# Optimization experiments

Hardware: AMD Instinct MI355X
Metric: run time of the kernel (lower is better)

The kernel has to match this reference:

```python
import jax, jax.numpy as jnp
import numpy as np

SHAPE = (8, 16, 16)          # N-dim spatial shape, seq_len = 2048
DIM_Q = 512
DIM_KV = 512
N_HEAD = 8
N_LAYER = 8
D_K = DIM_Q // N_HEAD        # 64
D_V = DIM_KV // N_HEAD       # 64


def setup_inputs() -> dict:
    key = jax.random.key(0)
    ks = jax.random.split(key, 8)
    b = 2
    q = jax.random.normal(ks[0], (b, *SHAPE, DIM_Q), dtype=jnp.float32)
    k = jax.random.normal(ks[1], (b, *SHAPE, DIM_KV), dtype=jnp.float32)
    v = jax.random.normal(ks[2], (b, *SHAPE, DIM_KV), dtype=jnp.float32)
    # torch nn.Linear weights are [out, in]; we apply x @ W.T below
    Wq = jax.random.normal(ks[3], (N_HEAD * D_K, DIM_Q), dtype=jnp.float32) / np.sqrt(DIM_Q)
    Wk = jax.random.normal(ks[4], (N_HEAD * D_K, DIM_KV), dtype=jnp.float32) / np.sqrt(DIM_KV)
    Wv = jax.random.normal(ks[5], (N_HEAD * D_V, DIM_KV), dtype=jnp.float32) / np.sqrt(DIM_KV)
    Wo = jax.random.normal(ks[6], (DIM_Q, N_HEAD * D_V), dtype=jnp.float32) / np.sqrt(DIM_Q * N_LAYER)
    bo = jnp.zeros((DIM_Q,), dtype=jnp.float32)
    return {"q": q, "k": k, "v": v, "Wq": Wq, "Wk": Wk, "Wv": Wv, "Wo": Wo, "bo": bo}


def reference(q, k, v, Wq, Wk, Wv, Wo, bo):
    b = q.shape[0]
    spatial = q.shape[1:-1]                      # (8,16,16)
    n = int(np.prod(spatial))                    # 2048
    # flatten spatial dims -> [b, N, c]
    qf = q.reshape(b, n, -1)
    kf = k.reshape(b, n, -1)
    vf = v.reshape(b, n, -1)
    # QKV projections (nn.Linear, bias=False): x @ W.T
    qp = jnp.einsum('bnc,dc->bnd', qf, Wq)
    kp = jnp.einsum('bnc,dc->bnd', kf, Wk)
    vp = jnp.einsum('bnc,dc->bnd', vf, Wv)
    # split heads -> [b, h, N, d]
    qh = qp.reshape(b, n, N_HEAD, D_K).transpose(0, 2, 1, 3)
    kh = kp.reshape(b, n, N_HEAD, D_K).transpose(0, 2, 1, 3)
    vh = vp.reshape(b, n, N_HEAD, D_V).transpose(0, 2, 1, 3)
    # full attention with causal tril mask, scale 1/sqrt(d_k)
    scores = jnp.einsum('bhqd,bhkd->bhqk', qh, kh) / np.sqrt(D_K)
    causal = jnp.tril(jnp.ones((n, n), dtype=bool))
    scores = jnp.where(causal, scores, -jnp.inf)
    attn = jax.nn.softmax(scores, axis=-1)       # attn_dropout=0.0 -> identity
    a = jnp.einsum('bhqk,bhkd->bhqd', attn, vh)
    # merge heads -> [b, N, h*d_v]
    a = a.transpose(0, 2, 1, 3).reshape(b, n, N_HEAD * D_V)
    # output projection (bias=True)
    out = jnp.einsum('bnd,cd->bnc', a, Wo) + bo
    return out.reshape(b, *spatial, DIM_Q)
```

## Files before the change

kernel.cpp:

```cpp
#include <hip/hip_runtime.h>
#include <hip/hip_bf16.h>

typedef __bf16 bf16_t;
typedef __attribute__((ext_vector_type(4))) __bf16 bf16x4;
typedef __attribute__((ext_vector_type(8))) __bf16 bf16x8;
typedef __attribute__((ext_vector_type(4))) float f32x4;

#define MFMA16(a, b, c) __builtin_amdgcn_mfma_f32_16x16x32_bf16((a), (b), (c), 0, 0, 0)
#define EXP2(x) __builtin_amdgcn_exp2f(x)

constexpr int NB   = 2;
constexpr int NH   = 8;
constexpr int NSEQ = 2048;
constexpr int CD   = 512;
constexpr int DH   = 64;
constexpr int MTOK = NB * NSEQ;

__device__ __forceinline__ bf16_t f2b(float x) { return (bf16_t)x; }

__global__ __launch_bounds__(256) void qkv_proj_kernel(
    const float* __restrict__ Xq, const float* __restrict__ Xk, const float* __restrict__ Xv,
    const float* __restrict__ Wq, const float* __restrict__ Wk, const float* __restrict__ Wv,
    bf16_t* __restrict__ Qp, bf16_t* __restrict__ Kf, bf16_t* __restrict__ Vf)
{
    __shared__ bf16_t Xs[64][72];
    __shared__ bf16_t Ws[64][72];

    const int z = blockIdx.z;
    const float* __restrict__ X = (z == 0) ? Xq : (z == 1) ? Xk : Xv;
    const float* __restrict__ W = (z == 0) ? Wq : (z == 1) ? Wk : Wv;
    bf16_t* __restrict__ Out    = (z == 0) ? Qp : (z == 1) ? Kf : Vf;

    const int tid  = threadIdx.x;
    const int lane = tid & 63;
    const int wid  = tid >> 6;
    const int lrow = lane & 15;
    const int lk   = (lane >> 4) * 8;
    const int m0w  = (wid >> 1) * 32;
    const int n0w  = (wid & 1) * 32;
    const int bm   = blockIdx.x * 64;
    const int bn   = blockIdx.y * 64;

    const int srow = tid >> 4;
    const int sc4  = (tid & 15) * 4;

    f32x4 xg[4], wg[4];
    #pragma unroll
    for (int rr = 0; rr < 4; ++rr) {
        int r = rr * 16 + srow;
        xg[rr] = *reinterpret_cast<const f32x4*>(X + (size_t)(bm + r) * CD + sc4);
        wg[rr] = *reinterpret_cast<const f32x4*>(W + (size_t)(bn + r) * CD + sc4);
    }

    f32x4 acc[2][2] = {};
    for (int k0 = 0; k0 < CD; k0 += 64) {
        #pragma unroll
        for (int rr = 0; rr < 4; ++rr) {
            int r = rr * 16 + srow;
            bf16x4 xb, wb;
            #pragma unroll
            for (int c = 0; c < 4; ++c) { xb[c] = f2b(xg[rr][c]); wb[c] = f2b(wg[rr][c]); }
            *reinterpret_cast<bf16x4*>(&Xs[r][sc4]) = xb;
            *reinterpret_cast<bf16x4*>(&Ws[r][sc4]) = wb;
        }
        __syncthreads();

        if (k0 + 64 < CD) {
            #pragma unroll
            for (int rr = 0; rr < 4; ++rr) {
                int r = rr * 16 + srow;
                xg[rr] = *reinterpret_cast<const f32x4*>(X + (size_t)(bm + r) * CD + k0 + 64 + sc4);
                wg[rr] = *reinterpret_cast<const f32x4*>(W + (size_t)(bn + r) * CD + k0 + 64 + sc4);
            }
        }

        #pragma unroll
        for (int kk = 0; kk < 2; ++kk) {
            int o = kk * 32 + lk;
            bf16x8 a0 = *reinterpret_cast<const bf16x8*>(&Xs[m0w + lrow][o]);
            bf16x8 a1 = *reinterpret_cast<const bf16x8*>(&Xs[m0w + 16 + lrow][o]);
            bf16x8 b0 = *reinterpret_cast<const bf16x8*>(&Ws[n0w + lrow][o]);
            bf16x8 b1 = *reinterpret_cast<const bf16x8*>(&Ws[n0w + 16 + lrow][o]);
            acc[0][0] = MFMA16(a0, b0, acc[0][0]);
            acc[0][1] = MFMA16(a0, b1, acc[0][1]);
            acc[1][0] = MFMA16(a1, b0, acc[1][0]);
            acc[1][1] = MFMA16(a1, b1, acc[1][1]);
        }
        __syncthreads();
    }

    if (z == 0) {
        #pragma unroll
        for (int f = 0; f < 2; ++f)
            #pragma unroll
            for (int gg = 0; gg < 2; ++gg)
                #pragma unroll
                for (int j = 0; j < 4; ++j) {
                    int row = bm + m0w + f * 16 + (lane >> 4) * 4 + j;
                    int col = bn + n0w + gg * 16 + lrow;
                    int b = row >> 11, n = row & (NSEQ - 1);
                    int h = col >> 6,  d = col & (DH - 1);
                    Out[(((size_t)(b * NH + h) * NSEQ) + n) * DH + d] = f2b(acc[f][gg][j]);
                }
    } else if (z == 1) {
        #pragma unroll
        for (int f = 0; f < 2; ++f)
            #pragma unroll
            for (int gg = 0; gg < 2; ++gg) {
                int rowb = bm + m0w + f * 16 + (lane >> 4) * 4;
                int col  = bn + n0w + gg * 16 + lrow;
                int bq = rowb >> 11;
                int h = col >> 6, d = col & (DH - 1);
                bf16_t* hb = Out + (size_t)(bq * NH + h) * NSEQ * DH;
                #pragma unroll
                for (int j = 0; j < 4; ++j) {
                    int n = (rowb + j) & (NSEQ - 1);
                    hb[((size_t)(n >> 4) * 2 + (d >> 5)) * 512 +
                       ((d >> 3) & 3) * 128 + (n & 15) * 8 + (d & 7)] = f2b(acc[f][gg][j]);
                }
            }
    } else {
        #pragma unroll
        for (int f = 0; f < 2; ++f)
            #pragma unroll
            for (int gg = 0; gg < 2; ++gg) {
                int rowb = bm + m0w + f * 16 + (lane >> 4) * 4;
                int col  = bn + n0w + gg * 16 + lrow;
                int bq = rowb >> 11;
                int n0 = rowb & (NSEQ - 1);
                int h = col >> 6, dv = col & (DH - 1);
                bf16_t* hb = Out + (size_t)(bq * NH + h) * NSEQ * DH;
                bf16x4 pk;
                #pragma unroll
                for (int j = 0; j < 4; ++j) pk[j] = f2b(acc[f][gg][j]);
                *reinterpret_cast<bf16x4*>(
                    &hb[((size_t)(n0 >> 5) * 4 + (dv >> 4)) * 512 +
                        ((n0 >> 3) & 3) * 128 + (dv & 15) * 8 + (n0 & 7)]) = pk;
            }
    }
}

__device__ __forceinline__ void attn_qblock(
    const bf16_t* __restrict__ Q, const bf16_t* __restrict__ K,
    const bf16_t* __restrict__ V, bf16_t* __restrict__ Aout,
    int b, int h, int p, int tid,
    char (*wreg)[8704], float (*sl)[32])
{
    const int lane = tid & 63;
    const int w    = tid >> 6;
    const int r    = lane & 15;
    const int g    = lane >> 4;
    const int qb   = p * 32;

    bf16_t* Pl = (bf16_t*)wreg[w];

    const float QS = 0.125f * 1.4426950408889634f;
    const float MSHIFT = 16.f;
    bf16x8 qf[2][2];
    #pragma unroll
    for (int f = 0; f < 2; ++f)
        #pragma unroll
        for (int dh = 0; dh < 2; ++dh) {
            bf16x8 t = *reinterpret_cast<const bf16x8*>(
                Q + (size_t)(qb + f * 16 + r) * DH + dh * 32 + g * 8);
            #pragma unroll
            for (int i = 0; i < 8; ++i) qf[f][dh][i] = f2b((float)t[i] * QS);
        }

    float l0 = 0.f, l1 = 0.f;
    f32x4 O[2][4] = {};

    const int T = (p + 2) >> 1;

    bf16x8 kc[4][2];
    if (w < T) {
        #pragma unroll
        for (int kk = 0; kk < 4; ++kk)
            #pragma unroll
            for (int dh = 0; dh < 2; ++dh)
                kc[kk][dh] = *reinterpret_cast<const bf16x8*>(
                    K + (((size_t)(w * 4 + kk) * 2 + dh) * 64 + lane) * 8);
    }

    for (int c = w; c < T; c += 4) {
        const int kb = c * 64;

        bf16x8 bv[4][2];
        #pragma unroll
        for (int df = 0; df < 4; ++df)
            #pragma unroll
            for (int ks = 0; ks < 2; ++ks)
                bv[df][ks] = *reinterpret_cast<const bf16x8*>(
                    V + (((size_t)(c * 2 + ks) * 4 + df) * 64 + lane) * 8);

        f32x4 s[2][4] = {};
        __builtin_amdgcn_s_setprio(1);
        #pragma unroll
        for (int kk = 0; kk < 4; ++kk) {
            s[0][kk] = MFMA16(kc[kk][0], qf[0][0], s[0][kk]);
            s[0][kk] = MFMA16(kc[kk][1], qf[0][1], s[0][kk]);
            s[1][kk] = MFMA16(kc[kk][0], qf[1][0], s[1][kk]);
            s[1][kk] = MFMA16(kc[kk][1], qf[1][1], s[1][kk]);
        }
        __builtin_amdgcn_s_setprio(0);

        bf16x8 kn[4][2];
        const int cn = c + 4;
        if (cn < T) {
            #pragma unroll
            for (int kk = 0; kk < 4; ++kk)
                #pragma unroll
                for (int dh = 0; dh < 2; ++dh)
                    kn[kk][dh] = *reinterpret_cast<const bf16x8*>(
                        K + (((size_t)(cn * 4 + kk) * 2 + dh) * 64 + lane) * 8);
        }

        if (kb + 63 > qb) {
            #pragma unroll
            for (int f = 0; f < 2; ++f) {
                const int qg = qb + f * 16 + r;
                #pragma unroll
                for (int kk = 0; kk < 4; ++kk)
                    #pragma unroll
                    for (int j = 0; j < 4; ++j) {
                        int kg = kb + kk * 16 + g * 4 + j;
                        if (kg > qg) s[f][kk][j] = -1e30f;
                    }
            }
        }

        #pragma unroll
        for (int kk = 0; kk < 4; ++kk)
            #pragma unroll
            for (int j = 0; j < 4; ++j) {
                float e0 = EXP2(s[0][kk][j] - MSHIFT);
                float e1 = EXP2(s[1][kk][j] - MSHIFT);
                s[0][kk][j] = e0; l0 += e0;
                s[1][kk][j] = e1; l1 += e1;
            }

        #pragma unroll
        for (int f = 0; f < 2; ++f)
            #pragma unroll
            for (int kk = 0; kk < 4; ++kk) {
                bf16x4 pk4;
                #pragma unroll
                for (int j = 0; j < 4; ++j) pk4[j] = f2b(s[f][kk][j]);
                *reinterpret_cast<bf16x4*>(&Pl[(size_t)(f * 16 + r) * 72 + kk * 16 + g * 4]) = pk4;
            }
        asm volatile("s_waitcnt lgkmcnt(0)" ::: "memory");

        bf16x8 pa0l = *reinterpret_cast<const bf16x8*>(&Pl[(size_t)r * 72 + g * 8]);
        bf16x8 pa1l = *reinterpret_cast<const bf16x8*>(&Pl[(size_t)(16 + r) * 72 + g * 8]);
        bf16x8 pa0h = *reinterpret_cast<const bf16x8*>(&Pl[(size_t)r * 72 + 32 + g * 8]);
        bf16x8 pa1h = *reinterpret_cast<const bf16x8*>(&Pl[(size_t)(16 + r) * 72 + 32 + g * 8]);
        __builtin_amdgcn_s_setprio(1);
        #pragma unroll
        for (int df = 0; df < 4; ++df) {
            O[0][df] = MFMA16(pa0l, bv[df][0], O[0][df]);
            O[1][df] = MFMA16(pa1l, bv[df][0], O[1][df]);
            O[0][df] = MFMA16(pa0h, bv[df][1], O[0][df]);
            O[1][df] = MFMA16(pa1h, bv[df][1], O[1][df]);
        }
        __builtin_amdgcn_s_setprio(0);

        #pragma unroll
        for (int kk = 0; kk < 4; ++kk) { kc[kk][0] = kn[kk][0]; kc[kk][1] = kn[kk][1]; }
    }

    l0 += __shfl_xor(l0, 16);
    l1 += __shfl_xor(l1, 16);
    l0 += __shfl_xor(l0, 32);
    l1 += __shfl_xor(l1, 32);

    float* sO = (float*)wreg[w];
    #pragma unroll
    for (int f = 0; f < 2; ++f)
        #pragma unroll
        for (int df = 0; df < 4; ++df)
            #pragma unroll
            for (int j = 0; j < 4; ++j)
                sO[(size_t)(f * 16 + g * 4 + j) * 68 + df * 16 + r] = O[f][df][j];
    if (lane < 16) { sl[w][r] = l0; sl[w][16 + r] = l1; }
    __syncthreads();

    {
        const int row = tid >> 3;
        const int c0  = (tid & 7) * 8;
        float lstar = sl[0][row] + sl[1][row] + sl[2][row] + sl[3][row];
        f32x4 acc0 = {}, acc1 = {};
        #pragma unroll
        for (int w2 = 0; w2 < 4; ++w2) {
            const float* po = (const float*)wreg[w2] + (size_t)row * 68 + c0;
            f32x4 o0 = *reinterpret_cast<const f32x4*>(po);
            f32x4 o1 = *reinterpret_cast<const f32x4*>(po + 4);
            #pragma unroll
            for (int cc = 0; cc < 4; ++cc) { acc0[cc] += o0[cc]; acc1[cc] += o1[cc]; }
        }
        float inv = 1.f / lstar;
        bf16x8 pk;
        #pragma unroll
        for (int cc = 0; cc < 4; ++cc) { pk[cc] = f2b(acc0[cc] * inv); pk[4 + cc] = f2b(acc1[cc] * inv); }
        *reinterpret_cast<bf16x8*>(Aout + ((size_t)b * NSEQ + qb + row) * CD + h * DH + c0) = pk;
    }
    __syncthreads();
}

__global__ __launch_bounds__(256, 2) void attn_kernel(
    const bf16_t* __restrict__ Qp, const bf16_t* __restrict__ Kf,
    const bf16_t* __restrict__ Vf, bf16_t* __restrict__ Aout)
{
    __shared__ __align__(16) char wreg[4][8704];
    __shared__ float sl[4][32];

    const int tid = threadIdx.x;
    const int bh = blockIdx.x;
    const int b = bh >> 3, h = bh & 7;
    const int pp = blockIdx.y;

    const bf16_t* Q = Qp + (size_t)bh * NSEQ * DH;
    const bf16_t* K = Kf + (size_t)bh * NSEQ * DH;
    const bf16_t* V = Vf + (size_t)bh * NSEQ * DH;

    attn_qblock(Q, K, V, Aout, b, h, 63 - pp, tid, wreg, sl);
    attn_qblock(Q, K, V, Aout, b, h, pp,      tid, wreg, sl);
}

__global__ __launch_bounds__(256) void out_proj_kernel(
    const bf16_t* __restrict__ A, const float* __restrict__ Wo,
    const float* __restrict__ bo, float* __restrict__ Out)
{
    __shared__ bf16_t As[64][72];
    __shared__ bf16_t Ws[64][72];

    const int tid  = threadIdx.x;
    const int lane = tid & 63;
    const int wid  = tid >> 6;
    const int lrow = lane & 15;
    const int lk   = (lane >> 4) * 8;
    const int m0w  = (wid >> 1) * 32;
    const int n0w  = (wid & 1) * 32;
    const int bm   = blockIdx.x * 64;
    const int bn   = blockIdx.y * 64;

    const int srow = tid >> 4;
    const int sc4  = (tid & 15) * 4;

    bf16x4 ag[4];
    f32x4  wg[4];
    #pragma unroll
    for (int rr = 0; rr < 4; ++rr) {
        int r = rr * 16 + srow;
        ag[rr] = *reinterpret_cast<const bf16x4*>(A  + (size_t)(bm + r) * CD + sc4);
        wg[rr] = *reinterpret_cast<const f32x4*>(Wo + (size_t)(bn + r) * CD + sc4);
    }

    f32x4 acc[2][2] = {};
    for (int k0 = 0; k0 < CD; k0 += 64) {
        #pragma unroll
        for (int rr = 0; rr < 4; ++rr) {
            int r = rr * 16 + srow;
            bf16x4 wb;
            #pragma unroll
            for (int c = 0; c < 4; ++c) wb[c] = f2b(wg[rr][c]);
            *reinterpret_cast<bf16x4*>(&As[r][sc4]) = ag[rr];
            *reinterpret_cast<bf16x4*>(&Ws[r][sc4]) = wb;
        }
        __syncthreads();

        if (k0 + 64 < CD) {
            #pragma unroll
            for (int rr = 0; rr < 4; ++rr) {
                int r = rr * 16 + srow;
                ag[rr] = *reinterpret_cast<const bf16x4*>(A  + (size_t)(bm + r) * CD + k0 + 64 + sc4);
                wg[rr] = *reinterpret_cast<const f32x4*>(Wo + (size_t)(bn + r) * CD + k0 + 64 + sc4);
            }
        }

        #pragma unroll
        for (int kk = 0; kk < 2; ++kk) {
            int o = kk * 32 + lk;
            bf16x8 a0 = *reinterpret_cast<const bf16x8*>(&As[m0w + lrow][o]);
            bf16x8 a1 = *reinterpret_cast<const bf16x8*>(&As[m0w + 16 + lrow][o]);
            bf16x8 b0 = *reinterpret_cast<const bf16x8*>(&Ws[n0w + lrow][o]);
            bf16x8 b1 = *reinterpret_cast<const bf16x8*>(&Ws[n0w + 16 + lrow][o]);
            acc[0][0] = MFMA16(a0, b0, acc[0][0]);
            acc[0][1] = MFMA16(a0, b1, acc[0][1]);
            acc[1][0] = MFMA16(a1, b0, acc[1][0]);
            acc[1][1] = MFMA16(a1, b1, acc[1][1]);
        }
        __syncthreads();
    }

    #pragma unroll
    for (int f = 0; f < 2; ++f)
        #pragma unroll
        for (int g = 0; g < 2; ++g)
            #pragma unroll
            for (int j = 0; j < 4; ++j) {
                int row = bm + m0w + f * 16 + (lane >> 4) * 4 + j;
                int col = bn + n0w + g * 16 + lrow;
                Out[(size_t)row * CD + col] = acc[f][g][j] + bo[col];
            }
}

__global__ __launch_bounds__(256) void copy16_kernel(
    const f32x4* __restrict__ src, f32x4* __restrict__ dst, int n16)
{
    int i = blockIdx.x * 256 + threadIdx.x;
    if (i < n16) dst[i] = src[i];
}

extern "C" void kernel_launch(void* const* d_in, const int* in_sizes, int n_in,
                              void* d_out, int out_size, void* d_ws, size_t ws_size,
                              hipStream_t stream)
{
    const float* q  = (const float*)d_in[0];
    const float* k  = (const float*)d_in[1];
    const float* v  = (const float*)d_in[2];
    const float* Wq = (const float*)d_in[3];
    const float* Wk = (const float*)d_in[4];
    const float* Wv = (const float*)d_in[5];
    const float* Wo = (const float*)d_in[6];
    const float* bo = (const float*)d_in[7];

    const size_t proj_elems = (size_t)MTOK * CD;
    const size_t proj_bytes = proj_elems * sizeof(bf16_t);

    if (ws_size >= 4 * proj_bytes) {
        bf16_t* Qp   = (bf16_t*)d_ws;
        bf16_t* Kf   = Qp + proj_elems;
        bf16_t* Vf   = Kf + proj_elems;
        bf16_t* Aout = Vf + proj_elems;

        qkv_proj_kernel<<<dim3(MTOK / 64, CD / 64, 3), 256, 0, stream>>>(
            q, k, v, Wq, Wk, Wv, Qp, Kf, Vf);
        attn_kernel<<<dim3(NB * NH, 32), 256, 0, stream>>>(Qp, Kf, Vf, Aout);
        out_proj_kernel<<<dim3(MTOK / 64, CD / 64), 256, 0, stream>>>(
            Aout, Wo, bo, (float*)d_out);
    } else {
        bf16_t* Qp   = (bf16_t*)d_out;
        bf16_t* Kf   = (bf16_t*)d_ws;
        bf16_t* Vf   = Kf + proj_elems;
        bf16_t* Atmp = Qp + proj_elems;
        bf16_t* Afin = (bf16_t*)d_ws;

        qkv_proj_kernel<<<dim3(MTOK / 64, CD / 64, 3), 256, 0, stream>>>(
            q, k, v, Wq, Wk, Wv, Qp, Kf, Vf);
        attn_kernel<<<dim3(NB * NH, 32), 256, 0, stream>>>(Qp, Kf, Vf, Atmp);
        const int n16 = (int)(proj_bytes / 16);
        copy16_kernel<<<dim3(n16 / 256), 256, 0, stream>>>(
            (const f32x4*)Atmp, (f32x4*)Afin, n16);
        out_proj_kernel<<<dim3(MTOK / 64, CD / 64), 256, 0, stream>>>(
            Afin, Wo, bo, (float*)d_out);
    }
}
```

Before: 50.31 us.

## Pre-convert QKV weights to bf16 MFMA-fragment layout and read directly from global

A new pre-pass kernel converts Wq/Wk/Wv from fp32 to bf16 and stores them in a tiled layout that matches the MFMA B-operand fragment order. The QKV projection then loads B fragments straight from global memory with contiguous per-lane 16-byte loads, instead of loading fp32 weights, converting them and staging them through shared memory. This halves weight bytes and drops the Ws shared tile and its conversion, at the cost of one extra launch and uncached-by-LDS global reads that are repeated across blocks. The converted weights live in the attention-output buffer, which is written only after the projection has finished.

```diff
diff --git a/kernel.cpp b/kernel.cpp
--- a/kernel.cpp
+++ b/kernel.cpp
@@ -15,20 +15,41 @@
 constexpr int CD   = 512;
 constexpr int DH   = 64;
 constexpr int MTOK = NB * NSEQ;
+constexpr int WELEM = CD * CD;
 
 __device__ __forceinline__ bf16_t f2b(float x) { return (bf16_t)x; }
+
+__global__ __launch_bounds__(256) void wconv_kernel(
+    const float* __restrict__ Wq, const float* __restrict__ Wk,
+    const float* __restrict__ Wv, bf16_t* __restrict__ Wf)
+{
+    const int z = blockIdx.y;
+    const float* __restrict__ W = (z == 0) ? Wq : (z == 1) ? Wk : Wv;
+    const int t  = blockIdx.x * 256 + threadIdx.x;
+    const int n  = t >> 6;
+    const int k8 = (t & 63) * 8;
+
+    f32x4 a = *reinterpret_cast<const f32x4*>(W + (size_t)n * CD + k8);
+    f32x4 b = *reinterpret_cast<const f32x4*>(W + (size_t)n * CD + k8 + 4);
+    bf16x8 r;
+    #pragma unroll
+    for (int i = 0; i < 4; ++i) { r[i] = f2b(a[i]); r[4 + i] = f2b(b[i]); }
+
+    *reinterpret_cast<bf16x8*>(
+        Wf + (size_t)z * WELEM +
+        ((size_t)(n >> 4) * 16 + (k8 >> 5)) * 512 + ((k8 >> 3) & 3) * 128 + (n & 15) * 8) = r;
+}
 
 __global__ __launch_bounds__(256) void qkv_proj_kernel(
     const float* __restrict__ Xq, const float* __restrict__ Xk, const float* __restrict__ Xv,
-    const float* __restrict__ Wq, const float* __restrict__ Wk, const float* __restrict__ Wv,
+    const bf16_t* __restrict__ Wf,
     bf16_t* __restrict__ Qp, bf16_t* __restrict__ Kf, bf16_t* __restrict__ Vf)
 {
     __shared__ bf16_t Xs[64][72];
-    __shared__ bf16_t Ws[64][72];
 
     const int z = blockIdx.z;
     const float* __restrict__ X = (z == 0) ? Xq : (z == 1) ? Xk : Xv;
-    const float* __restrict__ W = (z == 0) ? Wq : (z == 1) ? Wk : Wv;
+    const bf16_t* __restrict__ Wz = Wf + (size_t)z * WELEM;
     bf16_t* __restrict__ Out    = (z == 0) ? Qp : (z == 1) ? Kf : Vf;
 
     const int tid  = threadIdx.x;
@@ -43,13 +64,13 @@
 
     const int srow = tid >> 4;
     const int sc4  = (tid & 15) * 4;
-
-    f32x4 xg[4], wg[4];
+    const int nt0  = (bn + n0w) >> 4;
+
+    f32x4 xg[4];
     #pragma unroll
     for (int rr = 0; rr < 4; ++rr) {
         int r = rr * 16 + srow;
         xg[rr] = *reinterpret_cast<const f32x4*>(X + (size_t)(bm + r) * CD + sc4);
-        wg[rr] = *reinterpret_cast<const f32x4*>(W + (size_t)(bn + r) * CD + sc4);
     }
 
     f32x4 acc[2][2] = {};
@@ -57,11 +78,10 @@
         #pragma unroll
         for (int rr = 0; rr < 4; ++rr) {
             int r = rr * 16 + srow;
-            bf16x4 xb, wb;
-            #pragma unroll
-            for (int c = 0; c < 4; ++c) { xb[c] = f2b(xg[rr][c]); wb[c] = f2b(wg[rr][c]); }
+            bf16x4 xb;
+            #pragma unroll
+            for (int c = 0; c < 4; ++c) xb[c] = f2b(xg[rr][c]);
             *reinterpret_cast<bf16x4*>(&Xs[r][sc4]) = xb;
-            *reinterpret_cast<bf16x4*>(&Ws[r][sc4]) = wb;
         }
         __syncthreads();
 
@@ -70,17 +90,19 @@
             for (int rr = 0; rr < 4; ++rr) {
                 int r = rr * 16 + srow;
                 xg[rr] = *reinterpret_cast<const f32x4*>(X + (size_t)(bm + r) * CD + k0 + 64 + sc4);
-                wg[rr] = *reinterpret_cast<const f32x4*>(W + (size_t)(bn + r) * CD + k0 + 64 + sc4);
             }
         }
 
         #pragma unroll
         for (int kk = 0; kk < 2; ++kk) {
-            int o = kk * 32 + lk;
+            const int o  = kk * 32 + lk;
+            const int kt = (k0 >> 5) + kk;
             bf16x8 a0 = *reinterpret_cast<const bf16x8*>(&Xs[m0w + lrow][o]);
             bf16x8 a1 = *reinterpret_cast<const bf16x8*>(&Xs[m0w + 16 + lrow][o]);
-            bf16x8 b0 = *reinterpret_cast<const bf16x8*>(&Ws[n0w + lrow][o]);
-            bf16x8 b1 = *reinterpret_cast<const bf16x8*>(&Ws[n0w + 16 + lrow][o]);
+            bf16x8 b0 = *reinterpret_cast<const bf16x8*>(
+                Wz + ((size_t)nt0 * 16 + kt) * 512 + lane * 8);
+            bf16x8 b1 = *reinterpret_cast<const bf16x8*>(
+                Wz + ((size_t)(nt0 + 1) * 16 + kt) * 512 + lane * 8);
             acc[0][0] = MFMA16(a0, b0, acc[0][0]);
             acc[0][1] = MFMA16(a0, b1, acc[0][1]);
             acc[1][0] = MFMA16(a1, b0, acc[1][0]);
@@ -432,9 +454,10 @@
         bf16_t* Kf   = Qp + proj_elems;
         bf16_t* Vf   = Kf + proj_elems;
         bf16_t* Aout = Vf + proj_elems;
-
+        bf16_t* Wst  = Aout;
+        wconv_kernel<<<dim3(128, 3), 256, 0, stream>>>(Wq, Wk, Wv, Wst);
         qkv_proj_kernel<<<dim3(MTOK / 64, CD / 64, 3), 256, 0, stream>>>(
-            q, k, v, Wq, Wk, Wv, Qp, Kf, Vf);
+            q, k, v, Wst, Qp, Kf, Vf);
         attn_kernel<<<dim3(NB * NH, 32), 256, 0, stream>>>(Qp, Kf, Vf, Aout);
         out_proj_kernel<<<dim3(MTOK / 64, CD / 64), 256, 0, stream>>>(
             Aout, Wo, bo, (float*)d_out);
@@ -444,9 +467,10 @@
         bf16_t* Vf   = Kf + proj_elems;
         bf16_t* Atmp = Qp + proj_elems;
         bf16_t* Afin = (bf16_t*)d_ws;
-
+        bf16_t* Wst  = Atmp;
+        wconv_kernel<<<dim3(128, 3), 256, 0, stream>>>(Wq, Wk, Wv, Wst);
         qkv_proj_kernel<<<dim3(MTOK / 64, CD / 64, 3), 256, 0, stream>>>(
-            q, k, v, Wq, Wk, Wv, Qp, Kf, Vf);
+            q, k, v, Wst, Qp, Kf, Vf);
         attn_kernel<<<dim3(NB * NH, 32), 256, 0, stream>>>(Qp, Kf, Vf, Atmp);
         const int n16 = (int)(proj_bytes / 16);
         copy16_kernel<<<dim3(n16 / 256), 256, 0, stream>>>(
```

After: 55.20 us. 9.7% more time.
